# Kernel tuning notes

Measured on AMD Instinct MI355X. Metric: run time of the kernel, lower is better.

Reference implementation:

```python
import jax, jax.numpy as jnp
import numpy as np

D_EMB = 256


def setup_inputs() -> dict:
    key = jax.random.key(0)
    ks = jax.random.split(key, 7)
    B, S, d = 4, 4096, D_EMB
    scale = 1.0 / np.sqrt(d)
    return {
        "x": jax.random.normal(ks[0], (B, S, d), jnp.float32),
        "Wqkv": jax.random.normal(ks[1], (d, 3 * d), jnp.float32) * scale,
        "bqkv": jax.random.normal(ks[2], (3 * d,), jnp.float32) * 0.02,
        "Wproj": jax.random.normal(ks[3], (d, d), jnp.float32) * scale,
        "bproj": jax.random.normal(ks[4], (d,), jnp.float32) * 0.02,
        "Wfc": jax.random.normal(ks[5], (d, 1), jnp.float32) * scale,
        "bfc": jax.random.normal(ks[6], (1,), jnp.float32) * 0.02,
    }


def reference(x, Wqkv, bqkv, Wproj, bproj, Wfc, bfc):
    # qkv projection: [B,S,3d] -> split into q,k,v [B,S,d]
    qkv = x @ Wqkv + bqkv
    q, k, v = jnp.split(qkv, 3, axis=2)
    # full attention scores [B,S,S]; note: original applies NO 1/sqrt(d)
    # scaling (dead branch in source), 'traditional' softmax over last dim
    attn_scores = jnp.einsum("bqd,bkd->bqk", q, k)
    attn_weights = jax.nn.softmax(attn_scores, axis=-1)
    y = jnp.einsum("bqk,bkd->bqd", attn_weights, v)
    y = y @ Wproj + bproj
    out = y @ Wfc + bfc  # [B,S,1]
    return out
```

## Files before the change

kernel.cpp:

```cpp
#include <hip/hip_runtime.h>
#include <hip/hip_bf16.h>

#define BQ 4
#define SQ 4096
#define DQ 256
#define N3 768
#define KBLK 64
#define NITER (SQ / KBLK)
#define KHALF (NITER / 2)
#define LOG2E 1.44269504f
#define THR2 11.5415603f

typedef __attribute__((ext_vector_type(8))) _Float16 f16x8;
typedef __attribute__((ext_vector_type(4))) float f32x4;
typedef __attribute__((ext_vector_type(4))) unsigned int u32x4;

__device__ __forceinline__ short f2h(float f) {
  _Float16 h = (_Float16)f;
  union { _Float16 h; short s; } v; v.h = h;
  return v.s;
}

__device__ __forceinline__ void gload16(const void* g, void* lds) {
  __builtin_amdgcn_global_load_lds(
      (const __attribute__((address_space(1))) unsigned int*)g,
      (__attribute__((address_space(3))) unsigned int*)lds, 16, 0, 0);
}

__global__ void wcomb_kernel(const float* __restrict__ Wproj,
                             const float* __restrict__ bproj,
                             const float* __restrict__ Wfc,
                             const float* __restrict__ bfc,
                             float* __restrict__ Wc) {
  __shared__ float wf[256];
  const int t = threadIdx.x;
  wf[t] = Wfc[t];
  __syncthreads();
  float acc = 0.f;
  for (int j = 0; j < 256; ++j) acc += Wproj[(size_t)t * 256 + j] * wf[j];
  Wc[t] = acc;
  if (t == 0) {
    float c = bfc[0];
    for (int j = 0; j < 256; ++j) c += bproj[j] * wf[j];
    Wc[256] = c;
  }
}

__global__ void wconv_kernel(const float* __restrict__ Wqkv,
                             short* __restrict__ W16T) {
  __shared__ float tile[64][65];
  const int nb = blockIdx.x * 64;
  const int kb = blockIdx.y * 64;
  const int t = threadIdx.x;
  const int tr = t >> 6, tc = t & 63;
#pragma unroll
  for (int i = 0; i < 16; ++i)
    tile[tr + i * 4][tc] = Wqkv[(size_t)(kb + tr + i * 4) * N3 + nb + tc];
  __syncthreads();
#pragma unroll
  for (int i = 0; i < 16; ++i)
    W16T[(size_t)(nb + tr + i * 4) * 256 + kb + tc] = f2h(tile[tc][tr + i * 4]);
}

__global__ __launch_bounds__(1024, 4) void qkv_kernel(
    const float* __restrict__ x, const short* __restrict__ W16T,
    const float* __restrict__ bqkv, const float* __restrict__ Wc,
    short* __restrict__ Qb, short* __restrict__ Kb, float* __restrict__ u) {
  __shared__ short xs[64][264];
  __shared__ short ws[2][64][256];
  __shared__ float u_red[4][4][16];
  const int t = threadIdx.x;
  const int l = t & 63, w = t >> 6;
  const int lr = l & 15, lg = l >> 4;
  const int mq = w >> 2, nq = w & 3;
  const int Mbase = blockIdx.x * 64;

#define STAGE_W(BUF, NT)                                                      \
  {                                                                           \
    _Pragma("unroll") for (int i = 0; i < 2; ++i) {                           \
      const int n = w * 4 + i * 2 + (l >> 5);                                 \
      const int gc = (l & 31) ^ (n & 7);                                      \
      gload16(W16T + (size_t)((NT)*64 + n) * 256 + gc * 8,                    \
              &ws[BUF][w * 4 + i * 2][0]);                                    \
    }                                                                         \
  }

  STAGE_W(0, 0);

  {
    const int m = t >> 4, kc = (t & 15) * 16;
    const float* src = x + (size_t)(Mbase + m) * DQ + kc;
    short tmp[16];
#pragma unroll
    for (int i = 0; i < 16; ++i) tmp[i] = f2h(src[i]);
    *(u32x4*)&xs[m][kc] = *(u32x4*)&tmp[0];
    *(u32x4*)&xs[m][kc + 8] = *(u32x4*)&tmp[8];
  }

  float bias_qk[8], bias_u[4], wc_u[4];
#pragma unroll
  for (int i = 0; i < 8; ++i) bias_qk[i] = bqkv[i * 64 + nq * 16 + lr];
#pragma unroll
  for (int i = 0; i < 4; ++i) {
    bias_u[i] = bqkv[512 + i * 64 + nq * 16 + lr];
    wc_u[i] = Wc[i * 64 + nq * 16 + lr];
  }

  __syncthreads();

  unsigned qksto[8][2];
  float upart[4] = {0.f, 0.f, 0.f, 0.f};

#pragma unroll
  for (int nt = 0; nt < 12; ++nt) {
    const int cur = nt & 1;
    if (nt + 1 < 12) {
      STAGE_W(cur ^ 1, nt + 1);
      asm volatile("s_waitcnt vmcnt(2)" ::: "memory");
    } else {
      asm volatile("s_waitcnt vmcnt(0)" ::: "memory");
    }
    __builtin_amdgcn_s_barrier();
    __builtin_amdgcn_sched_barrier(0);

    f32x4 acc = {};
    const char* wR = (const char*)&ws[cur][nq * 16 + lr][0];
#pragma unroll
    for (int kk = 0; kk < 8; ++kk) {
      f16x8 af = *(f16x8*)&xs[mq * 16 + lr][kk * 32 + lg * 8];
      f16x8 bfr = *(const f16x8*)(wR + (((4 * kk + lg) ^ (lr & 7)) << 4));
      acc = __builtin_amdgcn_mfma_f32_16x16x32_f16(af, bfr, acc, 0, 0, 0);
    }
    if (nt < 8) {
      const float sc = (nt < 4) ? 1.f : LOG2E;
      unsigned s0 = (unsigned short)f2h((acc[0] + bias_qk[nt]) * sc);
      unsigned s1 = (unsigned short)f2h((acc[1] + bias_qk[nt]) * sc);
      unsigned s2 = (unsigned short)f2h((acc[2] + bias_qk[nt]) * sc);
      unsigned s3 = (unsigned short)f2h((acc[3] + bias_qk[nt]) * sc);
      qksto[nt][0] = s0 | (s1 << 16);
      qksto[nt][1] = s2 | (s3 << 16);
    } else {
#pragma unroll
      for (int r = 0; r < 4; ++r) upart[r] += (acc[r] + bias_u[nt - 8]) * wc_u[nt - 8];
    }
    __builtin_amdgcn_s_barrier();
  }

#pragma unroll
  for (int nt = 0; nt < 8; ++nt) {
    const int col = nt * 64 + nq * 16 + lr;
#pragma unroll
    for (int r = 0; r < 4; ++r) {
      const int row = Mbase + mq * 16 + lg * 4 + r;
      const short sv = (short)((qksto[nt][r >> 1] >> ((r & 1) * 16)) & 0xFFFF);
      if (col < 256) Qb[(size_t)row * DQ + col] = sv;
      else           Kb[(size_t)row * DQ + (col - 256)] = sv;
    }
  }

#pragma unroll
  for (int mask = 1; mask <= 8; mask <<= 1)
#pragma unroll
    for (int r = 0; r < 4; ++r) upart[r] += __shfl_xor(upart[r], mask, 64);
  if (lr == 0) {
#pragma unroll
    for (int r = 0; r < 4; ++r) u_red[mq][nq][lg * 4 + r] = upart[r];
  }
  __syncthreads();
  if (t < 64)
    u[Mbase + t] = u_red[t >> 4][0][t & 15] + u_red[t >> 4][1][t & 15] +
                   u_red[t >> 4][2][t & 15] + u_red[t >> 4][3][t & 15];
#undef STAGE_W
}

__global__ __launch_bounds__(512, 4) void attn_kernel(
    const short* __restrict__ Qb, const short* __restrict__ Kb,
    const float* __restrict__ u, float* __restrict__ Pm,
    float* __restrict__ Pd, float* __restrict__ Pn) {
  __shared__ short Ks[2][64][256];
  __shared__ __align__(16) float u_lds[2048];
  __shared__ float Mrg[2][4][32][3];

  const int t = threadIdx.x;
  const int l = t & 63, w = t >> 6;
  const int lr = l & 15, lg = l >> 4;
  const int qg = w >> 2, h = w & 3;
  const int bid = blockIdx.x;
  const int b = bid & 3;
  const int half = (bid >> 2) & 1;
  const int qbase = (bid >> 3) * 64;

  const short* kbase = Kb + ((size_t)b * SQ + (size_t)half * (SQ / 2)) * DQ;
  const float* ubase = u + (size_t)b * SQ + half * (SQ / 2);

#define STAGE(BUF, KB)                                                      \
  {                                                                         \
    _Pragma("unroll") for (int i = 0; i < 4; ++i) {                         \
      const int kr = w * 8 + i * 2 + (l >> 5);                              \
      const int gc = (l & 31) ^ (kr & 7);                                   \
      gload16(kbase + (size_t)((KB)*64 + kr) * DQ + gc * 8,                 \
              &Ks[BUF][w * 8 + i * 2][0]);                                  \
    }                                                                       \
  }

  STAGE(0, 0);
  gload16(ubase + w * 256 + (l << 2), &u_lds[w * 256]);

  f16x8 qf[2][8];
#pragma unroll
  for (int mm = 0; mm < 2; ++mm) {
    const short* qptr = Qb + (size_t)(b * SQ + qbase + qg * 32 + mm * 16 + lr) * DQ;
#pragma unroll
    for (int kk = 0; kk < 8; ++kk)
      qf[mm][kk] = *(const f16x8*)(qptr + kk * 32 + lg * 8);
  }

  float m_run[2] = {-1e30f, -1e30f};
  float num[2] = {0.f, 0.f}, den[2] = {0.f, 0.f};

  __syncthreads();

  for (int kb = 0; kb < KHALF; ++kb) {
    const int cur = kb & 1;
    if (kb + 1 < KHALF) {
      STAGE(cur ^ 1, kb + 1);
      asm volatile("s_waitcnt vmcnt(4)" ::: "memory");
    } else {
      asm volatile("s_waitcnt vmcnt(0)" ::: "memory");
    }
    __builtin_amdgcn_s_barrier();
    __builtin_amdgcn_sched_barrier(0);

    const char* kR = (const char*)&Ks[cur][h * 16 + lr][0];
    f32x4 s[2] = {};
    __builtin_amdgcn_s_setprio(1);
#pragma unroll
    for (int kk = 0; kk < 8; ++kk) {
      f16x8 kf = *(const f16x8*)(kR + (((4 * kk + lg) ^ (lr & 7)) << 4));
      s[0] = __builtin_amdgcn_mfma_f32_16x16x32_f16(kf, qf[0][kk], s[0], 0, 0, 0);
      s[1] = __builtin_amdgcn_mfma_f32_16x16x32_f16(kf, qf[1][kk], s[1], 0, 0, 0);
    }
    __builtin_amdgcn_s_setprio(0);

    bool over = false;
#pragma unroll
    for (int mm = 0; mm < 2; ++mm)
#pragma unroll
      for (int r = 0; r < 4; ++r) over = over || (s[mm][r] > m_run[mm] + THR2);
    if (__any(over)) {
#pragma unroll
      for (int mm = 0; mm < 2; ++mm) {
        float mt = fmaxf(fmaxf(s[mm][0], s[mm][1]), fmaxf(s[mm][2], s[mm][3]));
        mt = fmaxf(mt, __shfl_xor(mt, 16, 64));
        mt = fmaxf(mt, __shfl_xor(mt, 32, 64));
        const float mn = fmaxf(m_run[mm], mt);
        const float sc = exp2f(m_run[mm] - mn);
        m_run[mm] = mn;
        num[mm] *= sc;
        den[mm] *= sc;
      }
    }
    {
      const f32x4 uv = *(const f32x4*)&u_lds[kb * 64 + h * 16 + lg * 4];
#pragma unroll
      for (int mm = 0; mm < 2; ++mm)
#pragma unroll
        for (int r = 0; r < 4; ++r) {
          const float p = exp2f(s[mm][r] - m_run[mm]);
          den[mm] += p;
          num[mm] += p * uv[r];
        }
    }
    __builtin_amdgcn_s_barrier();
  }

#pragma unroll
  for (int mm = 0; mm < 2; ++mm) {
    num[mm] += __shfl_xor(num[mm], 16, 64);
    num[mm] += __shfl_xor(num[mm], 32, 64);
    den[mm] += __shfl_xor(den[mm], 16, 64);
    den[mm] += __shfl_xor(den[mm], 32, 64);
  }
  if (lg == 0) {
#pragma unroll
    for (int mm = 0; mm < 2; ++mm) {
      Mrg[qg][h][mm * 16 + lr][0] = m_run[mm];
      Mrg[qg][h][mm * 16 + lr][1] = den[mm];
      Mrg[qg][h][mm * 16 + lr][2] = num[mm];
    }
  }
  __syncthreads();

  if (t < 64) {
    const int row = t & 31, qg2 = t >> 5;
    float M = Mrg[qg2][0][row][0];
#pragma unroll
    for (int hh = 1; hh < 4; ++hh) M = fmaxf(M, Mrg[qg2][hh][row][0]);
    float dt = 0.f, nt = 0.f;
#pragma unroll
    for (int hh = 0; hh < 4; ++hh) {
      const float e = exp2f(Mrg[qg2][hh][row][0] - M);
      dt += e * Mrg[qg2][hh][row][1];
      nt += e * Mrg[qg2][hh][row][2];
    }
    const size_t idx = (size_t)half * (BQ * SQ) + (size_t)b * SQ + qbase + row +
                       qg2 * 32;
    Pm[idx] = M; Pd[idx] = dt; Pn[idx] = nt;
  }
#undef STAGE
}

__global__ void merge_kernel(const float* __restrict__ Pm,
                             const float* __restrict__ Pd,
                             const float* __restrict__ Pn,
                             const float* __restrict__ Wc,
                             float* __restrict__ out) {
  const int gid = blockIdx.x * 256 + threadIdx.x;
  const float m0 = Pm[gid], m1 = Pm[BQ * SQ + gid];
  const float M = fmaxf(m0, m1);
  const float e0 = exp2f(m0 - M), e1 = exp2f(m1 - M);
  const float den = e0 * Pd[gid] + e1 * Pd[BQ * SQ + gid];
  const float num = e0 * Pn[gid] + e1 * Pn[BQ * SQ + gid];
  out[gid] = num / den + Wc[256];
}

extern "C" void kernel_launch(void* const* d_in, const int* in_sizes, int n_in,
                              void* d_out, int out_size, void* d_ws, size_t ws_size,
                              hipStream_t stream) {
  const float* x     = (const float*)d_in[0];
  const float* Wqkv  = (const float*)d_in[1];
  const float* bqkv  = (const float*)d_in[2];
  const float* Wproj = (const float*)d_in[3];
  const float* bproj = (const float*)d_in[4];
  const float* Wfc   = (const float*)d_in[5];
  const float* bfc   = (const float*)d_in[6];
  float* out = (float*)d_out;

  const size_t SEG = (size_t)BQ * SQ * DQ * 2;
  char* wsb = (char*)d_ws;
  short* Qb   = (short*)(wsb);
  short* Kb   = (short*)(wsb + SEG);
  char* base  = wsb + 2 * SEG;
  float* Wc   = (float*)(base);
  float* u    = (float*)(base + 4096);
  short* W16T = (short*)(base + 4096 + 65536);
  float* Pm   = (float*)(base + 4096 + 65536 + 393216);
  float* Pd   = Pm + 2 * BQ * SQ;
  float* Pn   = Pd + 2 * BQ * SQ;

  wcomb_kernel<<<1, 256, 0, stream>>>(Wproj, bproj, Wfc, bfc, Wc);
  wconv_kernel<<<dim3(12, 4), 256, 0, stream>>>(Wqkv, W16T);
  qkv_kernel<<<256, 1024, 0, stream>>>(x, W16T, bqkv, Wc, Qb, Kb, u);
  attn_kernel<<<512, 512, 0, stream>>>(Qb, Kb, u, Pm, Pd, Pn);
  merge_kernel<<<BQ * SQ / 256, 256, 0, stream>>>(Pm, Pd, Pn, Wc, out);
}
```

Before: 105.8 us.

## Merge prep kernels, restructure attention K-staging barriers, use native exp2

Folds the weight-combine and weight-convert kernels into one launch, which removes a kernel launch. In the attention loop it waits for all loads, issues one barrier, then starts the next stage's prefetch, replacing the old partial vmcnt wait and trailing barrier. It also hoists the swizzled LDS offsets and computes the row max before the rescale check. exp2f becomes the hardware exp2 intrinsic, trading accuracy and denormal handling for fewer instructions. The reordered pipeline waits on vmcnt(0), so the prefetch overlaps less with the wait, and dropping the initial __syncthreads depends on the loop barrier for the u_lds load.

```diff
diff --git a/kernel.cpp b/kernel.cpp
--- a/kernel.cpp
+++ b/kernel.cpp
@@ -27,31 +27,29 @@
       (__attribute__((address_space(3))) unsigned int*)lds, 16, 0, 0);
 }
 
-__global__ void wcomb_kernel(const float* __restrict__ Wproj,
-                             const float* __restrict__ bproj,
-                             const float* __restrict__ Wfc,
-                             const float* __restrict__ bfc,
-                             float* __restrict__ Wc) {
-  __shared__ float wf[256];
+__global__ __launch_bounds__(256) void prep_kernel(
+    const float* __restrict__ Wqkv, const float* __restrict__ Wproj,
+    const float* __restrict__ bproj, const float* __restrict__ Wfc,
+    const float* __restrict__ bfc, short* __restrict__ W16T,
+    float* __restrict__ Wc) {
   const int t = threadIdx.x;
-  wf[t] = Wfc[t];
-  __syncthreads();
-  float acc = 0.f;
-  for (int j = 0; j < 256; ++j) acc += Wproj[(size_t)t * 256 + j] * wf[j];
-  Wc[t] = acc;
-  if (t == 0) {
-    float c = bfc[0];
-    for (int j = 0; j < 256; ++j) c += bproj[j] * wf[j];
-    Wc[256] = c;
-  }
-}
-
-__global__ void wconv_kernel(const float* __restrict__ Wqkv,
-                             short* __restrict__ W16T) {
+  if (blockIdx.x == 48) {
+    __shared__ float wf[256];
+    wf[t] = Wfc[t];
+    __syncthreads();
+    float acc = 0.f;
+    for (int j = 0; j < 256; ++j) acc += Wproj[(size_t)t * 256 + j] * wf[j];
+    Wc[t] = acc;
+    if (t == 0) {
+      float c = bfc[0];
+      for (int j = 0; j < 256; ++j) c += bproj[j] * wf[j];
+      Wc[256] = c;
+    }
+    return;
+  }
   __shared__ float tile[64][65];
-  const int nb = blockIdx.x * 64;
-  const int kb = blockIdx.y * 64;
-  const int t = threadIdx.x;
+  const int nb = (blockIdx.x % 12) * 64;
+  const int kb = (blockIdx.x / 12) * 64;
   const int tr = t >> 6, tc = t & 63;
 #pragma unroll
   for (int i = 0; i < 16; ++i)
@@ -215,46 +213,44 @@
       qf[mm][kk] = *(const f16x8*)(qptr + kk * 32 + lg * 8);
   }
 
+  int koff[8];
+#pragma unroll
+  for (int kk = 0; kk < 8; ++kk) koff[kk] = ((4 * kk + lg) ^ (lr & 7)) << 4;
+
   float m_run[2] = {-1e30f, -1e30f};
   float num[2] = {0.f, 0.f}, den[2] = {0.f, 0.f};
 
-  __syncthreads();
-
   for (int kb = 0; kb < KHALF; ++kb) {
     const int cur = kb & 1;
-    if (kb + 1 < KHALF) {
-      STAGE(cur ^ 1, kb + 1);
-      asm volatile("s_waitcnt vmcnt(4)" ::: "memory");
-    } else {
-      asm volatile("s_waitcnt vmcnt(0)" ::: "memory");
-    }
+    asm volatile("s_waitcnt vmcnt(0)" ::: "memory");
     __builtin_amdgcn_s_barrier();
     __builtin_amdgcn_sched_barrier(0);
+    if (kb + 1 < KHALF) STAGE(cur ^ 1, kb + 1);
 
     const char* kR = (const char*)&Ks[cur][h * 16 + lr][0];
     f32x4 s[2] = {};
     __builtin_amdgcn_s_setprio(1);
 #pragma unroll
     for (int kk = 0; kk < 8; ++kk) {
-      f16x8 kf = *(const f16x8*)(kR + (((4 * kk + lg) ^ (lr & 7)) << 4));
+      f16x8 kf = *(const f16x8*)(kR + koff[kk]);
       s[0] = __builtin_amdgcn_mfma_f32_16x16x32_f16(kf, qf[0][kk], s[0], 0, 0, 0);
       s[1] = __builtin_amdgcn_mfma_f32_16x16x32_f16(kf, qf[1][kk], s[1], 0, 0, 0);
     }
     __builtin_amdgcn_s_setprio(0);
 
-    bool over = false;
+    float mx[2];
 #pragma unroll
     for (int mm = 0; mm < 2; ++mm)
-#pragma unroll
-      for (int r = 0; r < 4; ++r) over = over || (s[mm][r] > m_run[mm] + THR2);
+      mx[mm] = fmaxf(fmaxf(s[mm][0], s[mm][1]), fmaxf(s[mm][2], s[mm][3]));
+    const bool over = (mx[0] > m_run[0] + THR2) || (mx[1] > m_run[1] + THR2);
     if (__any(over)) {
 #pragma unroll
       for (int mm = 0; mm < 2; ++mm) {
-        float mt = fmaxf(fmaxf(s[mm][0], s[mm][1]), fmaxf(s[mm][2], s[mm][3]));
+        float mt = mx[mm];
         mt = fmaxf(mt, __shfl_xor(mt, 16, 64));
         mt = fmaxf(mt, __shfl_xor(mt, 32, 64));
         const float mn = fmaxf(m_run[mm], mt);
-        const float sc = exp2f(m_run[mm] - mn);
+        const float sc = __builtin_amdgcn_exp2f(m_run[mm] - mn);
         m_run[mm] = mn;
         num[mm] *= sc;
         den[mm] *= sc;
@@ -266,12 +262,11 @@
       for (int mm = 0; mm < 2; ++mm)
 #pragma unroll
         for (int r = 0; r < 4; ++r) {
-          const float p = exp2f(s[mm][r] - m_run[mm]);
+          const float p = __builtin_amdgcn_exp2f(s[mm][r] - m_run[mm]);
           den[mm] += p;
           num[mm] += p * uv[r];
         }
     }
-    __builtin_amdgcn_s_barrier();
   }
 
 #pragma unroll
@@ -299,7 +294,7 @@
     float dt = 0.f, nt = 0.f;
 #pragma unroll
     for (int hh = 0; hh < 4; ++hh) {
-      const float e = exp2f(Mrg[qg2][hh][row][0] - M);
+      const float e = __builtin_amdgcn_exp2f(Mrg[qg2][hh][row][0] - M);
       dt += e * Mrg[qg2][hh][row][1];
       nt += e * Mrg[qg2][hh][row][2];
     }
@@ -318,7 +313,8 @@
   const int gid = blockIdx.x * 256 + threadIdx.x;
   const float m0 = Pm[gid], m1 = Pm[BQ * SQ + gid];
   const float M = fmaxf(m0, m1);
-  const float e0 = exp2f(m0 - M), e1 = exp2f(m1 - M);
+  const float e0 = __builtin_amdgcn_exp2f(m0 - M);
+  const float e1 = __builtin_amdgcn_exp2f(m1 - M);
   const float den = e0 * Pd[gid] + e1 * Pd[BQ * SQ + gid];
   const float num = e0 * Pn[gid] + e1 * Pn[BQ * SQ + gid];
   out[gid] = num / den + Wc[256];
@@ -348,8 +344,7 @@
   float* Pd   = Pm + 2 * BQ * SQ;
   float* Pn   = Pd + 2 * BQ * SQ;
 
-  wcomb_kernel<<<1, 256, 0, stream>>>(Wproj, bproj, Wfc, bfc, Wc);
-  wconv_kernel<<<dim3(12, 4), 256, 0, stream>>>(Wqkv, W16T);
+  prep_kernel<<<49, 256, 0, stream>>>(Wqkv, Wproj, bproj, Wfc, bfc, W16T, Wc);
   qkv_kernel<<<256, 1024, 0, stream>>>(x, W16T, bqkv, Wc, Qb, Kb, u);
   attn_kernel<<<512, 512, 0, stream>>>(Qb, Kb, u, Pm, Pd, Pn);
   merge_kernel<<<BQ * SQ / 256, 256, 0, stream>>>(Pm, Pd, Pn, Wc, out);
```

Measured after the change: 95.48 us. 9.8% less time.
